# Performance work log

Hardware: AMD Instinct MI355X
Metric: run time of the kernel (lower is better)

Reference implementation:

```python
import jax, jax.numpy as jnp
import numpy as np

K = 2
NOISE_STD = 1.0

def setup_inputs() -> dict:
    key = jax.random.key(0)
    k1, k2, k3 = jax.random.split(key, 3)
    N, D, E = 131072, 1024, 64
    x = jax.random.normal(k1, (N, D), dtype=jnp.float32)
    W = jax.random.normal(k2, (E, D), dtype=jnp.float32) * (1.0 / np.sqrt(D))
    b = jnp.zeros((E,), dtype=jnp.float32)
    noise = jax.random.normal(k3, (N, E), dtype=jnp.float32)
    return {"x": x, "W": W, "b": b, "noise": noise}

def reference(x, W, b, noise) -> jnp.ndarray:
    # clean logits: [N, E]
    clean_logits = jnp.einsum('nd,ed->ne', x, W) + b
    noisy_logits = clean_logits + noise * NOISE_STD
    topk_vals, topk_idx = jax.lax.top_k(noisy_logits, K)  # [N, K]
    topk_softmax = jax.nn.softmax(topk_vals, axis=-1)     # [N, K]
    rows = jnp.arange(x.shape[0])[:, None]                 # [N, 1]
    gate_weights = jnp.zeros_like(clean_logits).at[rows, topk_idx].set(topk_softmax)
    return gate_weights
```

## Files before the change

kernel.cpp:

```cpp
#include <hip/hip_runtime.h>
#include <math.h>


#define NEXP   64
#define BLOCK  256
#define TILE_M 128
#define KC     64
#define NCHUNK 16
#define KSTEPS 4
#define DFIX   1024
#define TAU    1e-3f
#define CAP    4096
#define WS_W_OFF 32768

typedef __attribute__((ext_vector_type(8)))  short bf16x8;
typedef __attribute__((ext_vector_type(16))) float f32x16;

__device__ __forceinline__ bool beats(float v, int e, float vo, int eo) {
    return (v > vo) || (v == vo && e < eo);
}

__device__ __forceinline__ void split2(float f0, float f1, unsigned int& hi, unsigned int& lo) {
    unsigned int u0 = __float_as_uint(f0), u1 = __float_as_uint(f1);
    unsigned int h0 = u0 & 0xFFFF0000u,  h1 = u1 & 0xFFFF0000u;
    float l0 = f0 - __uint_as_float(h0);
    float l1 = f1 - __uint_as_float(h1);
    hi = (u0 >> 16) | h1;
    lo = (__float_as_uint(l0) >> 16) | (__float_as_uint(l1) & 0xFFFF0000u);
}

__global__ void convW_kernel(const float* __restrict__ W, char* __restrict__ wsW) {
    const int e = blockIdx.x;
    const int t = threadIdx.x;
    const float* wp = W + e * DFIX + t * 8;
    float4 a  = *(const float4*)wp;
    float4 bq = *(const float4*)(wp + 4);
    unsigned int h[4], l[4];
    split2(a.x,  a.y,  h[0], l[0]);
    split2(a.z,  a.w,  h[1], l[1]);
    split2(bq.x, bq.y, h[2], l[2]);
    split2(bq.z, bq.w, h[3], l[3]);
    const int c   = t >> 3;
    const int ko  = t & 7;
    const int esw = e & 7;
    char* base = wsW + (size_t)c * 16384 + e * 256;
    *(uint4*)(base +       ((ko ^ esw) << 4)) = make_uint4(h[0], h[1], h[2], h[3]);
    *(uint4*)(base + 128 + ((ko ^ esw) << 4)) = make_uint4(l[0], l[1], l[2], l[3]);
}

__global__ __launch_bounds__(BLOCK, 4)
void gate_mfma(const float* __restrict__ x, const float* __restrict__ bvec,
               const float* __restrict__ noise, const char* __restrict__ wsW,
               float* __restrict__ out, unsigned int* __restrict__ flags) {
    __shared__ int4 wtile4[1024];
    char* wt = (char*)wtile4;

    const int tid  = threadIdx.x;
    const int wv   = tid >> 6;
    const int lane = tid & 63;
    const int e0   = lane & 31;
    const int lh   = lane >> 5;
    const int rowBase = blockIdx.x * TILE_M + wv * 32;

    const float* xrow = x + (size_t)(rowBase + e0) * DFIX;

    const int eA = e0, eB = e0 + 32;
    const int swA = eA & 7, swB = eB & 7;
    const int baseA = eA * 256, baseB = eB * 256;

    f32x16 acc0 = (f32x16)0.0f;
    f32x16 acc1 = (f32x16)0.0f;

    for (int c = 0; c < NCHUNK; c++) {
        __syncthreads();
        const char* src = wsW + (size_t)c * 16384;
        #pragma unroll
        for (int i = 0; i < 4; i++) {
            const int off = (tid + i * 256) * 16;
            *(int4*)(wt + off) = *(const int4*)(src + off);
        }
        __syncthreads();

        #pragma unroll
        for (int ks = 0; ks < KSTEPS; ks++) {
            const int koff = c * KC + ks * 16 + lh * 8;
            float4 xa = *(const float4*)(xrow + koff);
            float4 xb = *(const float4*)(xrow + koff + 4);
            union { bf16x8 v; unsigned int u[4]; } ah, al;
            split2(xa.x, xa.y, ah.u[0], al.u[0]);
            split2(xa.z, xa.w, ah.u[1], al.u[1]);
            split2(xb.x, xb.y, ah.u[2], al.u[2]);
            split2(xb.z, xb.w, ah.u[3], al.u[3]);

            const int slot = ks * 2 + lh;
            union { bf16x8 v; int4 q; } b0h, b0l, b1h, b1l;
            b0h.q = *(const int4*)(wt + baseA +       ((slot ^ swA) << 4));
            b0l.q = *(const int4*)(wt + baseA + 128 + ((slot ^ swA) << 4));
            b1h.q = *(const int4*)(wt + baseB +       ((slot ^ swB) << 4));
            b1l.q = *(const int4*)(wt + baseB + 128 + ((slot ^ swB) << 4));

            acc0 = __builtin_amdgcn_mfma_f32_32x32x16_bf16(ah.v, b0h.v, acc0, 0, 0, 0);
            acc1 = __builtin_amdgcn_mfma_f32_32x32x16_bf16(ah.v, b1h.v, acc1, 0, 0, 0);
            acc0 = __builtin_amdgcn_mfma_f32_32x32x16_bf16(ah.v, b0l.v, acc0, 0, 0, 0);
            acc1 = __builtin_amdgcn_mfma_f32_32x32x16_bf16(ah.v, b1l.v, acc1, 0, 0, 0);
            acc0 = __builtin_amdgcn_mfma_f32_32x32x16_bf16(al.v, b0h.v, acc0, 0, 0, 0);
            acc1 = __builtin_amdgcn_mfma_f32_32x32x16_bf16(al.v, b1h.v, acc1, 0, 0, 0);
        }
    }

    const float bb0 = bvec[e0], bb1 = bvec[e0 + 32];
    #pragma unroll
    for (int q = 0; q < 4; q++) {
        #pragma unroll
        for (int j = 0; j < 4; j++) {
            const int reg = q * 4 + j;
            const int r = rowBase + j + 8 * q + 4 * lh;
            const float n0 = noise[(size_t)r * NEXP + e0];
            const float n1 = noise[(size_t)r * NEXP + e0 + 32];
            const float v0 = (acc0[reg] + bb0) + n0;
            const float v1 = (acc1[reg] + bb1) + n1;

            float v1m, v2m, v3m = -1e30f; int e1m, e2m;
            if (beats(v0, e0, v1, e0 + 32)) { v1m = v0; e1m = e0;      v2m = v1; e2m = e0 + 32; }
            else                            { v1m = v1; e1m = e0 + 32; v2m = v0; e2m = e0;      }
            #pragma unroll
            for (int d = 1; d < 32; d <<= 1) {
                float ov1 = __shfl_xor(v1m, d); int oe1 = __shfl_xor(e1m, d);
                float ov2 = __shfl_xor(v2m, d); int oe2 = __shfl_xor(e2m, d);
                float ov3 = __shfl_xor(v3m, d);
                bool  aw  = beats(v1m, e1m, ov1, oe1);
                float a1v = aw ? v1m : ov1; int a1e = aw ? e1m : oe1;
                float b1v = aw ? ov1 : v1m; int b1e = aw ? oe1 : e1m;
                float a2v = aw ? v2m : ov2; int a2e = aw ? e2m : oe2;
                float b2v = aw ? ov2 : v2m;
                float a3v = aw ? v3m : ov3;
                bool  s2  = beats(a2v, a2e, b1v, b1e);
                v1m = a1v; e1m = a1e;
                v2m = s2 ? a2v : b1v; e2m = s2 ? a2e : b1e;
                v3m = s2 ? fmaxf(a3v, b1v) : fmaxf(a2v, b2v);
            }
            const float t   = __expf(v2m - v1m);
            const float inv = 1.0f / (1.0f + t);
            const float w1  = inv, w2 = t * inv;

            if (e0 == 0 && (v2m - v3m) < TAU) {
                unsigned int idx = atomicAdd(flags, 1u);
                if (idx < CAP) flags[1 + idx] = (unsigned int)r;
            }
            const int c0 = 2 * e0, c1 = c0 + 1;
            const float o0 = (c0 == e1m) ? w1 : (c0 == e2m) ? w2 : 0.0f;
            const float o1 = (c1 == e1m) ? w1 : (c1 == e2m) ? w2 : 0.0f;
            *(float2*)(out + (size_t)r * NEXP + c0) = make_float2(o0, o1);
        }
    }
}

__global__ void gate_repair(const float* __restrict__ x, const float* __restrict__ W,
                            const float* __restrict__ b, const float* __restrict__ noise,
                            float* __restrict__ out, const unsigned int* __restrict__ flags,
                            int D) {
    unsigned int cnt = flags[0];
    if (cnt > CAP) cnt = CAP;
    if (blockIdx.x >= cnt) return;
    const int r = (int)flags[1 + blockIdx.x];
    const int e = threadIdx.x;

    const float* xr = x + (size_t)r * D;
    const float* wr = W + (size_t)e * D;
    double s = 0.0;
    for (int d0 = 0; d0 < D; d0 += 4) {
        float4 xv = *(const float4*)(xr + d0);
        float4 wv = *(const float4*)(wr + d0);
        s += (double)xv.x * (double)wv.x;
        s += (double)xv.y * (double)wv.y;
        s += (double)xv.z * (double)wv.z;
        s += (double)xv.w * (double)wv.w;
    }
    const float clean = (float)s + b[e];
    const float v     = clean + noise[(size_t)r * NEXP + e];

    float v1 = v, v2 = -1e30f; int e1 = e, e2 = 99;
    for (int d = 1; d < 64; d <<= 1) {
        float ov1 = __shfl_xor(v1, d); int oe1 = __shfl_xor(e1, d);
        float ov2 = __shfl_xor(v2, d); int oe2 = __shfl_xor(e2, d);
        bool  aw  = beats(v1, e1, ov1, oe1);
        float a1v = aw ? v1 : ov1; int a1e = aw ? e1 : oe1;
        float b1v = aw ? ov1 : v1; int b1e = aw ? oe1 : e1;
        float a2v = aw ? v2 : ov2; int a2e = aw ? e2 : oe2;
        bool  s2  = beats(a2v, a2e, b1v, b1e);
        v1 = a1v; e1 = a1e;
        v2 = s2 ? a2v : b1v; e2 = s2 ? a2e : b1e;
    }
    const float t   = __expf(v2 - v1);
    const float inv = 1.0f / (1.0f + t);
    out[(size_t)r * NEXP + e] = (e == e1) ? inv : (e == e2) ? t * inv : 0.0f;
}

extern "C" void kernel_launch(void* const* d_in, const int* in_sizes, int n_in,
                              void* d_out, int out_size, void* d_ws, size_t ws_size,
                              hipStream_t stream) {
    const float* x     = (const float*)d_in[0];
    const float* W     = (const float*)d_in[1];
    const float* b     = (const float*)d_in[2];
    const float* noise = (const float*)d_in[3];
    float* out = (float*)d_out;

    const int E = in_sizes[2];
    const int D = in_sizes[1] / E;
    const int N = in_sizes[0] / D;

    unsigned int* flags = (unsigned int*)d_ws;
    char* wsW = (char*)d_ws + WS_W_OFF;

    convW_kernel<<<dim3(E), dim3(128), 0, stream>>>(W, wsW);
    hipMemsetAsync(d_ws, 0, sizeof(unsigned int), stream);
    gate_mfma<<<dim3(N / TILE_M), dim3(BLOCK), 0, stream>>>(x, b, noise, wsW, out, flags);
    gate_repair<<<dim3(CAP), dim3(64), 0, stream>>>(x, W, b, noise, out, flags, D);
}
```

Measured before the change: 233.6 us.

## Load pre-swizzled MFMA weight fragments directly from global, drop LDS staging

```diff
diff --git a/kernel.cpp b/kernel.cpp
--- a/kernel.cpp
+++ b/kernel.cpp
@@ -5,10 +5,8 @@
 #define NEXP   64
 #define BLOCK  256
 #define TILE_M 128
-#define KC     64
-#define NCHUNK 16
-#define KSTEPS 4
 #define DFIX   1024
+#define NKSTEP 64
 #define TAU    1e-3f
 #define CAP    4096
 #define WS_W_OFF 32768
@@ -40,21 +38,19 @@
     split2(a.z,  a.w,  h[1], l[1]);
     split2(bq.x, bq.y, h[2], l[2]);
     split2(bq.z, bq.w, h[3], l[3]);
-    const int c   = t >> 3;
-    const int ko  = t & 7;
-    const int esw = e & 7;
-    char* base = wsW + (size_t)c * 16384 + e * 256;
-    *(uint4*)(base +       ((ko ^ esw) << 4)) = make_uint4(h[0], h[1], h[2], h[3]);
-    *(uint4*)(base + 128 + ((ko ^ esw) << 4)) = make_uint4(l[0], l[1], l[2], l[3]);
+    const int kk   = t >> 1;
+    const int lh   = t & 1;
+    const int lane = lh * 32 + (e & 31);
+    const int g    = e >> 5;
+    char* base = wsW + (size_t)(kk * 4 + g * 2) * 1024 + lane * 16;
+    *(uint4*)(base)        = make_uint4(h[0], h[1], h[2], h[3]);
+    *(uint4*)(base + 1024) = make_uint4(l[0], l[1], l[2], l[3]);
 }
 
 __global__ __launch_bounds__(BLOCK, 4)
 void gate_mfma(const float* __restrict__ x, const float* __restrict__ bvec,
                const float* __restrict__ noise, const char* __restrict__ wsW,
                float* __restrict__ out, unsigned int* __restrict__ flags) {
-    __shared__ int4 wtile4[1024];
-    char* wt = (char*)wtile4;
-
     const int tid  = threadIdx.x;
     const int wv   = tid >> 6;
     const int lane = tid & 63;
@@ -62,50 +58,36 @@
     const int lh   = lane >> 5;
     const int rowBase = blockIdx.x * TILE_M + wv * 32;
 
-    const float* xrow = x + (size_t)(rowBase + e0) * DFIX;
-
-    const int eA = e0, eB = e0 + 32;
-    const int swA = eA & 7, swB = eB & 7;
-    const int baseA = eA * 256, baseB = eB * 256;
+    const float* xrow  = x + (size_t)(rowBase + e0) * DFIX + lh * 8;
+    const char*  wfrag = wsW + lane * 16;
 
     f32x16 acc0 = (f32x16)0.0f;
     f32x16 acc1 = (f32x16)0.0f;
 
-    for (int c = 0; c < NCHUNK; c++) {
-        __syncthreads();
-        const char* src = wsW + (size_t)c * 16384;
-        #pragma unroll
-        for (int i = 0; i < 4; i++) {
-            const int off = (tid + i * 256) * 16;
-            *(int4*)(wt + off) = *(const int4*)(src + off);
-        }
-        __syncthreads();
-
-        #pragma unroll
-        for (int ks = 0; ks < KSTEPS; ks++) {
-            const int koff = c * KC + ks * 16 + lh * 8;
-            float4 xa = *(const float4*)(xrow + koff);
-            float4 xb = *(const float4*)(xrow + koff + 4);
-            union { bf16x8 v; unsigned int u[4]; } ah, al;
-            split2(xa.x, xa.y, ah.u[0], al.u[0]);
-            split2(xa.z, xa.w, ah.u[1], al.u[1]);
-            split2(xb.x, xb.y, ah.u[2], al.u[2]);
-            split2(xb.z, xb.w, ah.u[3], al.u[3]);
-
-            const int slot = ks * 2 + lh;
-            union { bf16x8 v; int4 q; } b0h, b0l, b1h, b1l;
-            b0h.q = *(const int4*)(wt + baseA +       ((slot ^ swA) << 4));
-            b0l.q = *(const int4*)(wt + baseA + 128 + ((slot ^ swA) << 4));
-            b1h.q = *(const int4*)(wt + baseB +       ((slot ^ swB) << 4));
-            b1l.q = *(const int4*)(wt + baseB + 128 + ((slot ^ swB) << 4));
-
-            acc0 = __builtin_amdgcn_mfma_f32_32x32x16_bf16(ah.v, b0h.v, acc0, 0, 0, 0);
-            acc1 = __builtin_amdgcn_mfma_f32_32x32x16_bf16(ah.v, b1h.v, acc1, 0, 0, 0);
-            acc0 = __builtin_amdgcn_mfma_f32_32x32x16_bf16(ah.v, b0l.v, acc0, 0, 0, 0);
-            acc1 = __builtin_amdgcn_mfma_f32_32x32x16_bf16(ah.v, b1l.v, acc1, 0, 0, 0);
-            acc0 = __builtin_amdgcn_mfma_f32_32x32x16_bf16(al.v, b0h.v, acc0, 0, 0, 0);
-            acc1 = __builtin_amdgcn_mfma_f32_32x32x16_bf16(al.v, b1h.v, acc1, 0, 0, 0);
-        }
+    #pragma unroll 4
+    for (int kk = 0; kk < NKSTEP; kk++) {
+        const float4 xa = *(const float4*)(xrow + kk * 16);
+        const float4 xb = *(const float4*)(xrow + kk * 16 + 4);
+
+        const char* fb = wfrag + (size_t)(kk * 4) * 1024;
+        union { bf16x8 v; int4 q; } b0h, b0l, b1h, b1l;
+        b0h.q = *(const int4*)(fb);
+        b0l.q = *(const int4*)(fb + 1024);
+        b1h.q = *(const int4*)(fb + 2048);
+        b1l.q = *(const int4*)(fb + 3072);
+
+        union { bf16x8 v; unsigned int u[4]; } ah, al;
+        split2(xa.x, xa.y, ah.u[0], al.u[0]);
+        split2(xa.z, xa.w, ah.u[1], al.u[1]);
+        split2(xb.x, xb.y, ah.u[2], al.u[2]);
+        split2(xb.z, xb.w, ah.u[3], al.u[3]);
+
+        acc0 = __builtin_amdgcn_mfma_f32_32x32x16_bf16(ah.v, b0h.v, acc0, 0, 0, 0);
+        acc1 = __builtin_amdgcn_mfma_f32_32x32x16_bf16(ah.v, b1h.v, acc1, 0, 0, 0);
+        acc0 = __builtin_amdgcn_mfma_f32_32x32x16_bf16(ah.v, b0l.v, acc0, 0, 0, 0);
+        acc1 = __builtin_amdgcn_mfma_f32_32x32x16_bf16(ah.v, b1l.v, acc1, 0, 0, 0);
+        acc0 = __builtin_amdgcn_mfma_f32_32x32x16_bf16(al.v, b0h.v, acc0, 0, 0, 0);
+        acc1 = __builtin_amdgcn_mfma_f32_32x32x16_bf16(al.v, b1h.v, acc1, 0, 0, 0);
     }
 
     const float bb0 = bvec[e0], bb1 = bvec[e0 + 32];
```

Result: slower. 274.1 us (+17.4%).
